# Kernel tuning notes

Hardware: AMD Instinct MI355X
Metric: run time of the kernel (lower is better)

Reference implementation:

```python
import jax, jax.numpy as jnp
import numpy as np

B, T, P, D, S, R = 4, 128, 256, 512, 64, 8  # batch, window, patches, d_model, n_state, dt_rank


def setup_inputs() -> dict:
    key = jax.random.key(0)
    ks = jax.random.split(key, 8)
    sc = 0.02  # weight init scale
    return {
        "X": jax.random.normal(ks[0], (B, T, P, D), jnp.float32),
        "H0": jnp.zeros((B, P, S), jnp.float32),
        "a_hat": jax.random.normal(ks[1], (S,), jnp.float32),
        "U_w": jax.random.normal(ks[2], (S, D), jnp.float32) * sc,
        "sB_w": jax.random.normal(ks[3], (S, D), jnp.float32) * sc,
        "sB_b": jnp.zeros((S,), jnp.float32),
        "sC_w": jax.random.normal(ks[4], (S, D), jnp.float32) * sc,
        "sC_b": jnp.zeros((S,), jnp.float32),
        "sD1_w": jax.random.normal(ks[5], (R, D), jnp.float32) * sc,
        "sD1_b": jnp.zeros((R,), jnp.float32),
        "sD2_w": jax.random.normal(ks[6], (1, R), jnp.float32) * sc,
        "sD2_b": jnp.zeros((1,), jnp.float32),
        "ro_w": jax.random.normal(ks[7], (D, S), jnp.float32) * sc,
    }


def reference(X, H0, a_hat, U_w, sB_w, sB_b, sC_w, sC_b, sD1_w, sD1_b, sD2_w, sD2_b, ro_w):
    eps = 1e-12
    logA = -jnp.exp(a_hat)                                    # [S]
    # selective (input-dependent) parameters
    u = jnp.einsum('btpd,sd->btps', X, U_w)                   # [B,T,P,S]
    B_t = jnp.einsum('btpd,sd->btps', X, sB_w) + sB_b
    C_t = jnp.einsum('btpd,sd->btps', X, sC_w) + sC_b
    dt_feat = jax.nn.silu(jnp.einsum('btpd,rd->btpr', X, sD1_w) + sD1_b)
    dt = jax.nn.softplus(jnp.einsum('btpr,or->btpo', dt_feat, sD2_w) + sD2_b)  # [B,T,P,1]
    A = jnp.exp(dt * logA)                                    # [B,T,P,S] via broadcast
    b = (1.0 - A) * (B_t * u)
    # prefix-product scan: h_t = A_t*h_{t-1} + b_t  ->  h_t = P_t*(H0 + cumsum(b/P))
    Pc = jnp.cumprod(jnp.maximum(A, eps), axis=1)             # [B,T,P,S]
    invP = 1.0 / jnp.maximum(Pc, eps)
    c = jnp.cumsum(b * invP, axis=1)
    H_seq = Pc * (H0[:, None] + c)                            # [B,T,P,S]
    Y_seq = jnp.einsum('btps,ds->btpd', C_t * H_seq, ro_w)    # [B,T,P,D]
    Y_seq = Y_seq.reshape(X.shape[0], -1, X.shape[-1])        # [B, T*P, D]
    H_T = H_seq[:, -1]                                        # [B,P,S]
    return (H_seq, Y_seq, H_T)
```

## Files before the change

kernel.cpp:

```cpp
#include <hip/hip_runtime.h>
#include <hip/hip_bf16.h>
#include <math.h>

namespace {
constexpr int B_N = 4, T_N = 128, P_N = 256, D_N = 512, S_N = 64;
constexpr int NTH = 512;
constexpr int KC  = 32;
constexpr int NCH = D_N / KC;

constexpr int XS0_OFF = 0;
constexpr int WS0_OFF = 8192;
constexpr int XS1_OFF = 24576;
constexpr int WS1_OFF = 32768;
constexpr int BU_OFF  = 0;
constexpr int CH_OFF  = 16384;
constexpr int ROS0_OFF= 32768;
constexpr int ROS1_OFF= 0;
constexpr int DT_OFF  = 49152;
constexpr int LDS_BYTES = 49664;

constexpr int WIMG_ELEMS  = NCH * 256 * 32;
constexpr int ROIMG_ELEMS = 4 * 128 * 64;
}

typedef short bf16x8 __attribute__((ext_vector_type(8)));
typedef float f32x4  __attribute__((ext_vector_type(4)));

__device__ __forceinline__ unsigned short f2b(float f) {
    unsigned int x = __float_as_uint(f);
    return (unsigned short)((x + 0x7FFFu + ((x >> 16) & 1u)) >> 16);
}
__device__ __forceinline__ float b2f(unsigned short h) {
    return __uint_as_float(((unsigned int)h) << 16);
}
__device__ __forceinline__ unsigned int pk2(float lo, float hi) {
    union { __hip_bfloat162 h; unsigned int u; } cv;
    cv.h = __float22bfloat162_rn(float2{lo, hi});
    return cv.u;
}
__device__ __forceinline__ int swz32(int row, int col) {
    return row * 32 + (col ^ (((row >> 1) & 3) << 3));
}
__device__ __forceinline__ int swz64(int row, int col) {
    return row * 64 + (col ^ ((row & 7) << 3));
}
__device__ __forceinline__ void cvtstore8(unsigned short* dst, float4 a, float4 b) {
    uint4 r;
    r.x = pk2(a.x, a.y); r.y = pk2(a.z, a.w);
    r.z = pk2(b.x, b.y); r.w = pk2(b.z, b.w);
    *(uint4*)dst = r;
}
__device__ __forceinline__ void gload16(const void* g, void* l) {
    __builtin_amdgcn_global_load_lds(
        (const __attribute__((address_space(1))) unsigned int*)g,
        (__attribute__((address_space(3))) unsigned int*)l, 16, 0, 0);
}
#define CBAR(N) do { \
    __builtin_amdgcn_sched_barrier(0); \
    asm volatile("s_waitcnt vmcnt(" #N ") lgkmcnt(0)" ::: "memory"); \
    __builtin_amdgcn_s_barrier(); \
    __builtin_amdgcn_sched_barrier(0); \
} while (0)

__global__ __launch_bounds__(512) void mamba_prep(
    const float* __restrict__ U_w, const float* __restrict__ sB_w,
    const float* __restrict__ sC_w, const float* __restrict__ sD1_w,
    const float* __restrict__ ro_w,
    unsigned short* __restrict__ wImg, unsigned short* __restrict__ roImg)
{
    const int idx = blockIdx.x * 512 + threadIdx.x;
    if (idx < WIMG_ELEMS) {
        const int kc = idx >> 13, rem = idx & 8191, r = rem >> 5, c = rem & 31;
        float v = 0.0f;
        if (r < 192) {
            const int g = r >> 4, w = r & 15, tr = g % 3, sb = g / 3;
            const float* base = (tr == 0) ? U_w : (tr == 1) ? sB_w : sC_w;
            v = base[(size_t)(sb * 16 + w) * D_N + kc * KC + c];
        } else if (r < 200) {
            v = sD1_w[(size_t)(r - 192) * D_N + kc * KC + c];
        }
        wImg[kc * 8192 + swz32(r, c)] = f2b(v);
    } else if (idx < WIMG_ELEMS + ROIMG_ELEMS) {
        const int j = idx - WIMG_ELEMS;
        const int pp = j >> 13, rem = j & 8191, r = rem >> 6, c = rem & 63;
        roImg[pp * 8192 + swz64(r, c)] = f2b(ro_w[(size_t)(pp * 128 + r) * S_N + c]);
    }
}

__global__ __launch_bounds__(NTH, 4) void mamba_mfma(
    const float* __restrict__ X, const float* __restrict__ H0,
    const float* __restrict__ a_hat,
    const float* __restrict__ sB_b, const float* __restrict__ sC_b,
    const float* __restrict__ sD1_b, const float* __restrict__ sD2_w,
    const float* __restrict__ sD2_b,
    const unsigned short* __restrict__ wImg, const unsigned short* __restrict__ roImg,
    float* __restrict__ Hseq, float* __restrict__ Y, float* __restrict__ HT)
{
    __shared__ __align__(16) char smem[LDS_BYTES];
    float* DTB = (float*)(smem + DT_OFF);

    const int tid  = threadIdx.x;
    const int lane = tid & 63;
    const int wid  = tid >> 6;
    const int wm   = wid >> 2;
    const int wn   = wid & 3;
    const int l15  = lane & 15;
    const int lg   = lane >> 4;
    const int lane16 = lane * 16;
    const int b    = blockIdx.x >> 8;
    const int p    = blockIdx.x & 255;
    const char* wImgB  = (const char*)wImg;
    const char* roImgB = (const char*)roImg;

    const float la  = (tid < 64) ? -expf(a_hat[tid]) : 0.0f;
    const float h0v = (tid < 64) ? H0[((size_t)b * P_N + p) * S_N + tid] : 0.0f;

    f32x4 acc[4][3];
    f32x4 accdt;
    #pragma unroll
    for (int q = 0; q < 4; ++q) accdt[q] = 0.0f;
    #pragma unroll
    for (int mf = 0; mf < 4; ++mf)
        #pragma unroll
        for (int nf = 0; nf < 3; ++nf)
            #pragma unroll
            for (int q = 0; q < 4; ++q) acc[mf][nf][q] = 0.0f;

    const int xr = tid >> 2, xq = tid & 3;
    const float* xsrc = X + (((size_t)b * T_N + xr) * P_N + p) * D_N + xq * 8;
    const int xoff = swz32(xr, xq * 8);

    float4 xe0, xe1, xo0, xo1;
    {
        float4 t0 = *(const float4*)(xsrc), t1 = *(const float4*)(xsrc + 4);
        cvtstore8((unsigned short*)(smem + XS0_OFF) + xoff, t0, t1);
        gload16(wImgB + wid * 2048 + lane16,        smem + WS0_OFF + wid * 2048);
        gload16(wImgB + wid * 2048 + 1024 + lane16, smem + WS0_OFF + wid * 2048 + 1024);
        __builtin_amdgcn_sched_barrier(0);
        const float* n1 = xsrc + 1 * KC;
        xo0 = *(const float4*)(n1); xo1 = *(const float4*)(n1 + 4);
        const float* n2 = xsrc + 2 * KC;
        xe0 = *(const float4*)(n2); xe1 = *(const float4*)(n2 + 4);
    }
    CBAR(4);

    const int kb = lg * 8;
    #pragma unroll 2
    for (int kc = 0; kc < 13; ++kc) {
        unsigned short* XSc = (unsigned short*)(smem + ((kc & 1) ? XS1_OFF : XS0_OFF));
        unsigned short* WSc = (unsigned short*)(smem + ((kc & 1) ? WS1_OFF : WS0_OFF));
        char*           XSn = smem + ((kc & 1) ? XS0_OFF : XS1_OFF);
        char*           WSn = smem + ((kc & 1) ? WS0_OFF : WS1_OFF);
        if ((kc + 1) & 1) cvtstore8((unsigned short*)XSn + xoff, xo0, xo1);
        else              cvtstore8((unsigned short*)XSn + xoff, xe0, xe1);
        gload16(wImgB + (kc + 1) * 16384 + wid * 2048 + lane16,        WSn + wid * 2048);
        gload16(wImgB + (kc + 1) * 16384 + wid * 2048 + 1024 + lane16, WSn + wid * 2048 + 1024);
        __builtin_amdgcn_sched_barrier(0);
        {
            const float* nx = xsrc + (kc + 3) * KC;
            if ((kc + 1) & 1) { xo0 = *(const float4*)(nx); xo1 = *(const float4*)(nx + 4); }
            else              { xe0 = *(const float4*)(nx); xe1 = *(const float4*)(nx + 4); }
        }
        __builtin_amdgcn_s_setprio(1);
        bf16x8 a[4];
        #pragma unroll
        for (int mf = 0; mf < 4; ++mf)
            a[mf] = *(const bf16x8*)&XSc[swz32(wm * 64 + mf * 16 + l15, kb)];
        #pragma unroll
        for (int nf = 0; nf < 3; ++nf) {
            bf16x8 bb = *(const bf16x8*)&WSc[swz32(wn * 48 + nf * 16 + l15, kb)];
            #pragma unroll
            for (int mf = 0; mf < 4; ++mf)
                acc[mf][nf] = __builtin_amdgcn_mfma_f32_16x16x32_bf16(a[mf], bb, acc[mf][nf], 0, 0, 0);
        }
        {
            bf16x8 adt = *(const bf16x8*)&XSc[swz32(wid * 16 + l15, kb)];
            bf16x8 bd  = *(const bf16x8*)&WSc[swz32(192 + l15, kb)];
            accdt = __builtin_amdgcn_mfma_f32_16x16x32_bf16(adt, bd, accdt, 0, 0, 0);
        }
        __builtin_amdgcn_s_setprio(0);
        CBAR(2);
    }
    for (int kc = 13; kc < NCH; ++kc) {
        unsigned short* XSc = (unsigned short*)(smem + ((kc & 1) ? XS1_OFF : XS0_OFF));
        unsigned short* WSc = (unsigned short*)(smem + ((kc & 1) ? WS1_OFF : WS0_OFF));
        char*           XSn = smem + ((kc & 1) ? XS0_OFF : XS1_OFF);
        char*           WSn = smem + ((kc & 1) ? WS0_OFF : WS1_OFF);
        if (kc + 1 < NCH) {
            if ((kc + 1) & 1) cvtstore8((unsigned short*)XSn + xoff, xo0, xo1);
            else              cvtstore8((unsigned short*)XSn + xoff, xe0, xe1);
            gload16(wImgB + (kc + 1) * 16384 + wid * 2048 + lane16,        WSn + wid * 2048);
            gload16(wImgB + (kc + 1) * 16384 + wid * 2048 + 1024 + lane16, WSn + wid * 2048 + 1024);
        }
        __builtin_amdgcn_s_setprio(1);
        bf16x8 a[4];
        #pragma unroll
        for (int mf = 0; mf < 4; ++mf)
            a[mf] = *(const bf16x8*)&XSc[swz32(wm * 64 + mf * 16 + l15, kb)];
        #pragma unroll
        for (int nf = 0; nf < 3; ++nf) {
            bf16x8 bb = *(const bf16x8*)&WSc[swz32(wn * 48 + nf * 16 + l15, kb)];
            #pragma unroll
            for (int mf = 0; mf < 4; ++mf)
                acc[mf][nf] = __builtin_amdgcn_mfma_f32_16x16x32_bf16(a[mf], bb, acc[mf][nf], 0, 0, 0);
        }
        {
            bf16x8 adt = *(const bf16x8*)&XSc[swz32(wid * 16 + l15, kb)];
            bf16x8 bd  = *(const bf16x8*)&WSc[swz32(192 + l15, kb)];
            accdt = __builtin_amdgcn_mfma_f32_16x16x32_bf16(adt, bd, accdt, 0, 0, 0);
        }
        __builtin_amdgcn_s_setprio(0);
        __syncthreads();
    }

    {
        unsigned short* BU  = (unsigned short*)(smem + BU_OFF);
        unsigned short* CHB = (unsigned short*)(smem + CH_OFF);
        const int s = wn * 16 + l15;
        const float biasB = sB_b[s], biasC = sC_b[s];
        #pragma unroll
        for (int mf = 0; mf < 4; ++mf) {
            #pragma unroll
            for (int q = 0; q < 4; ++q) {
                const int t = wm * 64 + mf * 16 + lg * 4 + q;
                const float u  = acc[mf][0][q];
                const float Bv = acc[mf][1][q] + biasB;
                const float Cv = acc[mf][2][q] + biasC;
                BU[t * 64 + s]   = f2b(Bv * u);
                CHB[swz64(t, s)] = f2b(Cv);
            }
        }
    }
    {
        const float w2 = (l15 < 8) ? sD2_w[l15] : 0.0f;
        const float b1 = (l15 < 8) ? sD1_b[l15] : 0.0f;
        const float b2 = sD2_b[0];
        #pragma unroll
        for (int q = 0; q < 4; ++q) {
            float z = accdt[q] + b1;
            float w = (z / (1.0f + expf(-z))) * w2;
            w = (l15 < 8) ? w : 0.0f;
            w += __shfl_xor(w, 1);
            w += __shfl_xor(w, 2);
            w += __shfl_xor(w, 4);
            if (l15 == 0) {
                float zz = w + b2;
                DTB[wid * 16 + lg * 4 + q] = (zz > 20.0f) ? zz : log1pf(expf(zz));
            }
        }
    }
    __syncthreads();

    if (tid < 64) {
        unsigned short* BU  = (unsigned short*)(smem + BU_OFF);
        unsigned short* CHB = (unsigned short*)(smem + CH_OFF);
        const int s = tid;
        float Pcv = 1.0f, cv = 0.0f, Hv = 0.0f;
        float* hout = Hseq + ((size_t)b * T_N * P_N + p) * S_N + s;
        for (int t = 0; t < T_N; ++t) {
            const float Av = expf(DTB[t] * la);
            const float bv = (1.0f - Av) * b2f(BU[t * 64 + s]);
            Pcv *= fmaxf(Av, 1e-12f);
            cv += bv * (1.0f / fmaxf(Pcv, 1e-12f));
            Hv = Pcv * (h0v + cv);
            hout[(size_t)t * P_N * S_N] = Hv;
            const int e = swz64(t, s);
            CHB[e] = f2b(b2f(CHB[e]) * Hv);
        }
        HT[((size_t)b * P_N + p) * S_N + s] = Hv;
    } else {
        for (int seg = wid - 1; seg < 16; seg += 7)
            gload16(roImgB + seg * 1024 + lane16, smem + ROS0_OFF + seg * 1024);
    }
    __syncthreads();

    bf16x8 af0[4], af1[4];
    {
        unsigned short* CHB = (unsigned short*)(smem + CH_OFF);
        #pragma unroll
        for (int mf = 0; mf < 4; ++mf) {
            af0[mf] = *(const bf16x8*)&CHB[swz64(wm * 64 + mf * 16 + l15, lg * 8)];
            af1[mf] = *(const bf16x8*)&CHB[swz64(wm * 64 + mf * 16 + l15, 32 + lg * 8)];
        }
    }

    for (int pp = 0; pp < 4; ++pp) {
        unsigned short* cur = (unsigned short*)(smem + ((pp & 1) ? ROS1_OFF : ROS0_OFF));
        char*           nxt = smem + ((pp & 1) ? ROS0_OFF : ROS1_OFF);
        if (pp < 3) {
            gload16(roImgB + (pp + 1) * 16384 + wid * 2048 + lane16,        nxt + wid * 2048);
            gload16(roImgB + (pp + 1) * 16384 + wid * 2048 + 1024 + lane16, nxt + wid * 2048 + 1024);
        }
        f32x4 yacc[4][2];
        #pragma unroll
        for (int mf = 0; mf < 4; ++mf)
            #pragma unroll
            for (int nf = 0; nf < 2; ++nf)
                #pragma unroll
                for (int q = 0; q < 4; ++q) yacc[mf][nf][q] = 0.0f;
        #pragma unroll
        for (int nf = 0; nf < 2; ++nf) {
            bf16x8 bb0 = *(const bf16x8*)&cur[swz64(wn * 32 + nf * 16 + l15, lg * 8)];
            bf16x8 bb1 = *(const bf16x8*)&cur[swz64(wn * 32 + nf * 16 + l15, 32 + lg * 8)];
            #pragma unroll
            for (int mf = 0; mf < 4; ++mf) {
                yacc[mf][nf] = __builtin_amdgcn_mfma_f32_16x16x32_bf16(af0[mf], bb0, yacc[mf][nf], 0, 0, 0);
                yacc[mf][nf] = __builtin_amdgcn_mfma_f32_16x16x32_bf16(af1[mf], bb1, yacc[mf][nf], 0, 0, 0);
            }
        }
        #pragma unroll
        for (int mf = 0; mf < 4; ++mf) {
            const int t0 = wm * 64 + mf * 16 + lg * 4;
            float* ybase = Y + (((size_t)b * T_N + t0) * P_N + p) * D_N + pp * 128 + wn * 32 + l15;
            #pragma unroll
            for (int nf = 0; nf < 2; ++nf) {
                #pragma unroll
                for (int q = 0; q < 4; ++q)
                    ybase[(size_t)q * P_N * D_N + nf * 16] = yacc[mf][nf][q];
            }
        }
        if (pp < 3) __syncthreads();
    }
}

extern "C" void kernel_launch(void* const* d_in, const int* in_sizes, int n_in,
                              void* d_out, int out_size, void* d_ws, size_t ws_size,
                              hipStream_t stream) {
    const float* X     = (const float*)d_in[0];
    const float* H0    = (const float*)d_in[1];
    const float* a_hat = (const float*)d_in[2];
    const float* U_w   = (const float*)d_in[3];
    const float* sB_w  = (const float*)d_in[4];
    const float* sB_b  = (const float*)d_in[5];
    const float* sC_w  = (const float*)d_in[6];
    const float* sC_b  = (const float*)d_in[7];
    const float* sD1_w = (const float*)d_in[8];
    const float* sD1_b = (const float*)d_in[9];
    const float* sD2_w = (const float*)d_in[10];
    const float* sD2_b = (const float*)d_in[11];
    const float* ro_w  = (const float*)d_in[12];

    float* out   = (float*)d_out;
    float* HseqP = out;
    float* YP    = out + (size_t)B_N * T_N * P_N * S_N;
    float* HTP   = YP  + (size_t)B_N * T_N * P_N * D_N;

    unsigned short* wImg  = (unsigned short*)d_ws;
    unsigned short* roImg = (unsigned short*)((char*)d_ws + 262144);

    hipLaunchKernelGGL(mamba_prep, dim3((WIMG_ELEMS + ROIMG_ELEMS) / 512), dim3(512), 0, stream,
                       U_w, sB_w, sC_w, sD1_w, ro_w, wImg, roImg);
    hipLaunchKernelGGL(mamba_mfma, dim3(B_N * P_N), dim3(NTH), 0, stream,
                       X, H0, a_hat, sB_b, sC_b, sD1_b, sD2_w, sD2_b,
                       wImg, roImg, HseqP, YP, HTP);
}
```

Before: 159.8 us.

## Simplify X prefetch, batch scan loads, vectorize C*H and Y stores

Several changes at once. The GEMM main loop drops the custom waitcnt barrier and the two-deep odd/even X register prefetch in favour of a single-stage prefetch inside one uniform loop. The serial scan now reads B*u and dt in blocks of four and writes H back into the BU buffer, and a separate parallel pass across all threads multiplies C by H using 16-byte LDS accesses. The readout MFMA swaps its operands so each lane holds four consecutive d values and can write Y with float4 stores instead of scalar strided stores. Losing the deeper prefetch may expose more global load latency in the main GEMM loop.

```diff
diff --git a/kernel.cpp b/kernel.cpp
--- a/kernel.cpp
+++ b/kernel.cpp
@@ -55,12 +55,6 @@
         (const __attribute__((address_space(1))) unsigned int*)g,
         (__attribute__((address_space(3))) unsigned int*)l, 16, 0, 0);
 }
-#define CBAR(N) do { \
-    __builtin_amdgcn_sched_barrier(0); \
-    asm volatile("s_waitcnt vmcnt(" #N ") lgkmcnt(0)" ::: "memory"); \
-    __builtin_amdgcn_s_barrier(); \
-    __builtin_amdgcn_sched_barrier(0); \
-} while (0)
 
 __global__ __launch_bounds__(512) void mamba_prep(
     const float* __restrict__ U_w, const float* __restrict__ sB_w,
@@ -130,67 +124,32 @@
     const float* xsrc = X + (((size_t)b * T_N + xr) * P_N + p) * D_N + xq * 8;
     const int xoff = swz32(xr, xq * 8);
 
-    float4 xe0, xe1, xo0, xo1;
+    float4 xA, xB;
     {
         float4 t0 = *(const float4*)(xsrc), t1 = *(const float4*)(xsrc + 4);
         cvtstore8((unsigned short*)(smem + XS0_OFF) + xoff, t0, t1);
         gload16(wImgB + wid * 2048 + lane16,        smem + WS0_OFF + wid * 2048);
         gload16(wImgB + wid * 2048 + 1024 + lane16, smem + WS0_OFF + wid * 2048 + 1024);
-        __builtin_amdgcn_sched_barrier(0);
-        const float* n1 = xsrc + 1 * KC;
-        xo0 = *(const float4*)(n1); xo1 = *(const float4*)(n1 + 4);
-        const float* n2 = xsrc + 2 * KC;
-        xe0 = *(const float4*)(n2); xe1 = *(const float4*)(n2 + 4);
-    }
-    CBAR(4);
+        const float* n1 = xsrc + KC;
+        xA = *(const float4*)(n1); xB = *(const float4*)(n1 + 4);
+    }
+    __syncthreads();
 
     const int kb = lg * 8;
     #pragma unroll 2
-    for (int kc = 0; kc < 13; ++kc) {
-        unsigned short* XSc = (unsigned short*)(smem + ((kc & 1) ? XS1_OFF : XS0_OFF));
-        unsigned short* WSc = (unsigned short*)(smem + ((kc & 1) ? WS1_OFF : WS0_OFF));
-        char*           XSn = smem + ((kc & 1) ? XS0_OFF : XS1_OFF);
-        char*           WSn = smem + ((kc & 1) ? WS0_OFF : WS1_OFF);
-        if ((kc + 1) & 1) cvtstore8((unsigned short*)XSn + xoff, xo0, xo1);
-        else              cvtstore8((unsigned short*)XSn + xoff, xe0, xe1);
-        gload16(wImgB + (kc + 1) * 16384 + wid * 2048 + lane16,        WSn + wid * 2048);
-        gload16(wImgB + (kc + 1) * 16384 + wid * 2048 + 1024 + lane16, WSn + wid * 2048 + 1024);
-        __builtin_amdgcn_sched_barrier(0);
-        {
-            const float* nx = xsrc + (kc + 3) * KC;
-            if ((kc + 1) & 1) { xo0 = *(const float4*)(nx); xo1 = *(const float4*)(nx + 4); }
-            else              { xe0 = *(const float4*)(nx); xe1 = *(const float4*)(nx + 4); }
-        }
-        __builtin_amdgcn_s_setprio(1);
-        bf16x8 a[4];
-        #pragma unroll
-        for (int mf = 0; mf < 4; ++mf)
-            a[mf] = *(const bf16x8*)&XSc[swz32(wm * 64 + mf * 16 + l15, kb)];
-        #pragma unroll
-        for (int nf = 0; nf < 3; ++nf) {
-            bf16x8 bb = *(const bf16x8*)&WSc[swz32(wn * 48 + nf * 16 + l15, kb)];
-            #pragma unroll
-            for (int mf = 0; mf < 4; ++mf)
-                acc[mf][nf] = __builtin_amdgcn_mfma_f32_16x16x32_bf16(a[mf], bb, acc[mf][nf], 0, 0, 0);
-        }
-        {
-            bf16x8 adt = *(const bf16x8*)&XSc[swz32(wid * 16 + l15, kb)];
-            bf16x8 bd  = *(const bf16x8*)&WSc[swz32(192 + l15, kb)];
-            accdt = __builtin_amdgcn_mfma_f32_16x16x32_bf16(adt, bd, accdt, 0, 0, 0);
-        }
-        __builtin_amdgcn_s_setprio(0);
-        CBAR(2);
-    }
-    for (int kc = 13; kc < NCH; ++kc) {
+    for (int kc = 0; kc < NCH; ++kc) {
         unsigned short* XSc = (unsigned short*)(smem + ((kc & 1) ? XS1_OFF : XS0_OFF));
         unsigned short* WSc = (unsigned short*)(smem + ((kc & 1) ? WS1_OFF : WS0_OFF));
         char*           XSn = smem + ((kc & 1) ? XS0_OFF : XS1_OFF);
         char*           WSn = smem + ((kc & 1) ? WS0_OFF : WS1_OFF);
         if (kc + 1 < NCH) {
-            if ((kc + 1) & 1) cvtstore8((unsigned short*)XSn + xoff, xo0, xo1);
-            else              cvtstore8((unsigned short*)XSn + xoff, xe0, xe1);
+            cvtstore8((unsigned short*)XSn + xoff, xA, xB);
             gload16(wImgB + (kc + 1) * 16384 + wid * 2048 + lane16,        WSn + wid * 2048);
             gload16(wImgB + (kc + 1) * 16384 + wid * 2048 + 1024 + lane16, WSn + wid * 2048 + 1024);
+        }
+        if (kc + 2 < NCH) {
+            const float* nx = xsrc + (kc + 2) * KC;
+            xA = *(const float4*)(nx); xB = *(const float4*)(nx + 4);
         }
         __builtin_amdgcn_s_setprio(1);
         bf16x8 a[4];
@@ -252,25 +211,59 @@
     __syncthreads();
 
     if (tid < 64) {
-        unsigned short* BU  = (unsigned short*)(smem + BU_OFF);
-        unsigned short* CHB = (unsigned short*)(smem + CH_OFF);
+        unsigned short* BU = (unsigned short*)(smem + BU_OFF);
         const int s = tid;
         float Pcv = 1.0f, cv = 0.0f, Hv = 0.0f;
         float* hout = Hseq + ((size_t)b * T_N * P_N + p) * S_N + s;
-        for (int t = 0; t < T_N; ++t) {
-            const float Av = expf(DTB[t] * la);
-            const float bv = (1.0f - Av) * b2f(BU[t * 64 + s]);
-            Pcv *= fmaxf(Av, 1e-12f);
-            cv += bv * (1.0f / fmaxf(Pcv, 1e-12f));
-            Hv = Pcv * (h0v + cv);
-            hout[(size_t)t * P_N * S_N] = Hv;
-            const int e = swz64(t, s);
-            CHB[e] = f2b(b2f(CHB[e]) * Hv);
+        float bn[4], dn[4];
+        #pragma unroll
+        for (int q = 0; q < 4; ++q) { bn[q] = b2f(BU[q * 64 + s]); dn[q] = DTB[q]; }
+        for (int t0 = 0; t0 < T_N; t0 += 4) {
+            float bc[4], dc[4];
+            #pragma unroll
+            for (int q = 0; q < 4; ++q) { bc[q] = bn[q]; dc[q] = dn[q]; }
+            if (t0 + 4 < T_N) {
+                #pragma unroll
+                for (int q = 0; q < 4; ++q) {
+                    bn[q] = b2f(BU[(t0 + 4 + q) * 64 + s]);
+                    dn[q] = DTB[t0 + 4 + q];
+                }
+            }
+            #pragma unroll
+            for (int q = 0; q < 4; ++q) {
+                const int t = t0 + q;
+                const float Av = expf(dc[q] * la);
+                const float bv = (1.0f - Av) * bc[q];
+                Pcv *= fmaxf(Av, 1e-12f);
+                cv += bv * (1.0f / fmaxf(Pcv, 1e-12f));
+                Hv = Pcv * (h0v + cv);
+                hout[(size_t)t * P_N * S_N] = Hv;
+                BU[t * 64 + s] = f2b(Hv);
+            }
         }
         HT[((size_t)b * P_N + p) * S_N + s] = Hv;
     } else {
         for (int seg = wid - 1; seg < 16; seg += 7)
             gload16(roImgB + seg * 1024 + lane16, smem + ROS0_OFF + seg * 1024);
+    }
+    __syncthreads();
+
+    {
+        unsigned short* BU  = (unsigned short*)(smem + BU_OFF);
+        unsigned short* CHB = (unsigned short*)(smem + CH_OFF);
+        const int r = tid >> 2, c0 = (tid & 3) * 16;
+        bf16x8 h0 = *(const bf16x8*)&BU[r * 64 + c0];
+        bf16x8 h1 = *(const bf16x8*)&BU[r * 64 + c0 + 8];
+        bf16x8 c8a = *(const bf16x8*)&CHB[swz64(r, c0)];
+        bf16x8 c8b = *(const bf16x8*)&CHB[swz64(r, c0 + 8)];
+        bf16x8 o0, o1;
+        #pragma unroll
+        for (int j = 0; j < 8; ++j) {
+            o0[j] = (short)f2b(b2f((unsigned short)c8a[j]) * b2f((unsigned short)h0[j]));
+            o1[j] = (short)f2b(b2f((unsigned short)c8b[j]) * b2f((unsigned short)h1[j]));
+        }
+        *(bf16x8*)&CHB[swz64(r, c0)]     = o0;
+        *(bf16x8*)&CHB[swz64(r, c0 + 8)] = o1;
     }
     __syncthreads();
 
@@ -304,19 +297,19 @@
             bf16x8 bb1 = *(const bf16x8*)&cur[swz64(wn * 32 + nf * 16 + l15, 32 + lg * 8)];
             #pragma unroll
             for (int mf = 0; mf < 4; ++mf) {
-                yacc[mf][nf] = __builtin_amdgcn_mfma_f32_16x16x32_bf16(af0[mf], bb0, yacc[mf][nf], 0, 0, 0);
-                yacc[mf][nf] = __builtin_amdgcn_mfma_f32_16x16x32_bf16(af1[mf], bb1, yacc[mf][nf], 0, 0, 0);
+                yacc[mf][nf] = __builtin_amdgcn_mfma_f32_16x16x32_bf16(bb0, af0[mf], yacc[mf][nf], 0, 0, 0);
+                yacc[mf][nf] = __builtin_amdgcn_mfma_f32_16x16x32_bf16(bb1, af1[mf], yacc[mf][nf], 0, 0, 0);
             }
         }
         #pragma unroll
         for (int mf = 0; mf < 4; ++mf) {
-            const int t0 = wm * 64 + mf * 16 + lg * 4;
-            float* ybase = Y + (((size_t)b * T_N + t0) * P_N + p) * D_N + pp * 128 + wn * 32 + l15;
+            const int t = wm * 64 + mf * 16 + l15;
+            float* ybase = Y + (((size_t)b * T_N + t) * P_N + p) * D_N;
             #pragma unroll
             for (int nf = 0; nf < 2; ++nf) {
-                #pragma unroll
-                for (int q = 0; q < 4; ++q)
-                    ybase[(size_t)q * P_N * D_N + nf * 16] = yacc[mf][nf][q];
+                const int d = pp * 128 + wn * 32 + nf * 16 + lg * 4;
+                *(float4*)(ybase + d) = make_float4(yacc[mf][nf][0], yacc[mf][nf][1],
+                                                    yacc[mf][nf][2], yacc[mf][nf][3]);
             }
         }
         if (pp < 3) __syncthreads();
```

Measured after the change: 155.3 us. -2.8%, faster.
